# Kernel tuning notes

Hardware: AMD Instinct MI355X
Metric: run time of the kernel (lower is better)

The kernel has to match this reference:

```python
import jax, jax.numpy as jnp
import numpy as np

GRID = 12  # sqrt(144), seq_len = 144 fixed by w_g shape


def _relative_position(n: int) -> jnp.ndarray:
    # grid cell centers for an n x n grid, flattened row-major -> (n*n,)
    idx = np.arange(n * n)
    row, col = idx // n, idx % n
    cx = (col + 0.5) / n  # (x_min + x_max)/2 with x_min=col/n, x_max=(col+1)/n
    cy = (row + 0.5) / n
    dx = cx[:, None] - cx[None, :]
    dy = cy[:, None] - cy[None, :]
    ax = np.sign(dx) * 0.5
    ay = np.sign(dy) * 0.5
    dx = np.abs(np.log(np.abs(dx) + 0.5))
    dy = np.abs(np.log(np.abs(dy) + 0.5))
    # cat along leading dim then permute(1,2,0) == stack last-dim in order (dx,dy,ax,ay)
    pos = np.stack([dx, dy, ax, ay], axis=-1).astype(np.float32)  # (S,S,4)
    return jnp.asarray(pos)


def setup_inputs() -> dict:
    key = jax.random.key(0)
    ks = jax.random.split(key, 9)
    B, S, D = 128, GRID * GRID, 1024
    sc = 1.0 / np.sqrt(D)
    return {
        "query": jax.random.normal(ks[0], (B, S, D), jnp.float32),
        "key": jax.random.normal(ks[1], (B, S, D), jnp.float32),
        "value": jax.random.normal(ks[2], (B, S, D), jnp.float32),
        "Wq": jax.random.normal(ks[3], (D, D), jnp.float32) * sc,
        "bq": jnp.zeros((D,), jnp.float32),
        "Wk": jax.random.normal(ks[4], (D, D), jnp.float32) * sc,
        "bk": jnp.zeros((D,), jnp.float32),
        "Wv": jax.random.normal(ks[5], (D, D), jnp.float32) * sc,
        "bv": jnp.zeros((D,), jnp.float32),
        "Wlin": jax.random.normal(ks[6], (D, 4), jnp.float32) * 0.5,
        "w_g": jax.random.normal(ks[7], (S, D, 1), jnp.float32) * sc,
    }


def reference(query, key, value, Wq, bq, Wk, bk, Wv, bv, Wlin, w_g):
    d_model = query.shape[-1]
    # QKV projections + ReLU activation (dropout is identity at eval)
    q = jax.nn.relu(jnp.einsum("bsd,ed->bse", query, Wq) + bq)
    k = jax.nn.relu(jnp.einsum("bsd,ed->bse", key, Wk) + bk)
    v = jax.nn.relu(jnp.einsum("bsd,ed->bse", value, Wv) + bv)
    # raw scores: (B, S, S)
    att = jnp.einsum("bsd,btd->bst", q, k) * (d_model ** -0.5)
    # relative-position bias: (S, S, 4) -> linear -> relu -> per-row w_g -> relu
    pos = _relative_position(GRID)
    rp = jax.nn.relu(jnp.einsum("stf,df->std", pos, Wlin))  # (S, S, D)
    rp = jax.nn.relu(jnp.einsum("std,sdo->sto", rp, w_g)[..., 0])  # (S, S)
    att = jax.nn.softmax(att + rp[None, :, :], axis=-1)
    return jnp.einsum("bst,btd->bsd", att, v)
```

## Files before the change

### kernel.cpp

```cpp
#include <hip/hip_runtime.h>
#include <hip/hip_fp16.h>

#define DEV __device__ __forceinline__

using half8 = __attribute__((ext_vector_type(8))) _Float16;
using half4 = __attribute__((ext_vector_type(4))) _Float16;
using f32x4 = __attribute__((ext_vector_type(4))) float;

DEV void gload_lds16(const void* g, void* l) {
  __builtin_amdgcn_global_load_lds((const __attribute__((address_space(1))) unsigned int*)g,
                                   (__attribute__((address_space(3))) unsigned int*)l,
                                   16, 0, 0);
}

DEV f32x4 mfma16x32(half8 a, half8 b, f32x4 c) {
  return __builtin_amdgcn_mfma_f32_16x16x32_f16(a, b, c, 0, 0, 0);
}

DEV void conv2048(const float* __restrict__ s, _Float16* __restrict__ d, int t) {
  int i = t * 8;
  float4 a = *(const float4*)(s + i);
  float4 b = *(const float4*)(s + i + 4);
  half8 h;
  h[0] = (_Float16)a.x; h[1] = (_Float16)a.y; h[2] = (_Float16)a.z; h[3] = (_Float16)a.w;
  h[4] = (_Float16)b.x; h[5] = (_Float16)b.y; h[6] = (_Float16)b.z; h[7] = (_Float16)b.w;
  *(half8*)(d + i) = h;
}

DEV void rp_body(const float* __restrict__ Wlin, const float* __restrict__ wg,
                 float* __restrict__ rp, int s, int t) {
  if (t >= 144) return;
  int rs = s / 12, cs = s % 12, rt = t / 12, ct = t % 12;
  float dx = (cs - ct) / 12.f, dy = (rs - rt) / 12.f;
  float ax = (dx > 0.f) ? 0.5f : (dx < 0.f ? -0.5f : 0.f);
  float ay = (dy > 0.f) ? 0.5f : (dy < 0.f ? -0.5f : 0.f);
  float lx = fabsf(logf(fabsf(dx) + 0.5f));
  float ly = fabsf(logf(fabsf(dy) + 0.5f));
  float a0 = 0.f, a1 = 0.f, a2 = 0.f, a3 = 0.f;
  const float* wgs = wg + s * 1024;
  for (int d = 0; d < 1024; d += 4) {
#pragma unroll
    for (int u = 0; u < 4; ++u) {
      float4 w = *(const float4*)(Wlin + (d + u) * 4);
      float dot = lx * w.x + ly * w.y + ax * w.z + ay * w.w;
      dot = dot > 0.f ? dot : 0.f;
      float p = dot * wgs[d + u];
      if (u == 0) a0 += p; else if (u == 1) a1 += p; else if (u == 2) a2 += p; else a3 += p;
    }
  }
  float acc = (a0 + a1) + (a2 + a3);
  rp[s * 144 + t] = acc > 0.f ? acc : 0.f;
}

__global__ void prep_all(const float* __restrict__ query, const float* __restrict__ key,
                         const float* __restrict__ value, _Float16* __restrict__ ia,
                         _Float16* __restrict__ ib, _Float16* __restrict__ ic,
                         const float* __restrict__ Wq, const float* __restrict__ Wk,
                         const float* __restrict__ Wv, _Float16* __restrict__ Wqb,
                         _Float16* __restrict__ Wkb, _Float16* __restrict__ Wvb,
                         const float* __restrict__ Wlin, const float* __restrict__ wg,
                         float* __restrict__ rp, _Float16* __restrict__ vt) {
  int id = blockIdx.x, t = threadIdx.x;
  if (id < 144) {
    rp_body(Wlin, wg, rp, id, t);
  } else if (id < 656) {
    int i = (id - 144) * 256 + t;
    _Float16* p = vt + (size_t)i * 160 + 144;
    *(half8*)p = (half8){};
    *(half8*)(p + 8) = (half8){};
  } else if (id < 2192) {
    int id3 = id - 656;
    int z = id3 >> 9, r = id3 & 511;
    const float* s = z == 0 ? Wq : (z == 1 ? Wk : Wv);
    _Float16* d = z == 0 ? Wqb : (z == 1 ? Wkb : Wvb);
    conv2048(s + r * 2048, d + r * 2048, t);
  } else {
    int id4 = id - 2192;
    int z = id4 / 9216, r = id4 % 9216;
    const float* s = z == 0 ? query : (z == 1 ? key : value);
    _Float16* d = z == 0 ? ia : (z == 1 ? ib : ic);
    conv2048(s + (size_t)r * 2048, d + (size_t)r * 2048, t);
  }
}

__global__ void prep_small(const float* __restrict__ Wq, const float* __restrict__ Wk,
                           const float* __restrict__ Wv, _Float16* __restrict__ Wqb,
                           _Float16* __restrict__ Wkb, _Float16* __restrict__ Wvb,
                           const float* __restrict__ Wlin, const float* __restrict__ wg,
                           float* __restrict__ rp, _Float16* __restrict__ vt) {
  int id = blockIdx.x, t = threadIdx.x;
  if (id < 144) {
    rp_body(Wlin, wg, rp, id, t);
  } else if (id < 656) {
    int i = (id - 144) * 256 + t;
    _Float16* p = vt + (size_t)i * 160 + 144;
    *(half8*)p = (half8){};
    *(half8*)(p + 8) = (half8){};
  } else {
    int id3 = id - 656;
    int z = id3 >> 9, r = id3 & 511;
    const float* s = z == 0 ? Wq : (z == 1 ? Wk : Wv);
    _Float16* d = z == 0 ? Wqb : (z == 1 ? Wkb : Wvb);
    conv2048(s + r * 2048, d + r * 2048, t);
  }
}

__global__ void conv3_f32_f16(const float* __restrict__ s0, const float* __restrict__ s1,
                              const float* __restrict__ s2, _Float16* __restrict__ d0,
                              _Float16* __restrict__ d1, _Float16* __restrict__ d2, int n) {
  const float* s = blockIdx.z == 0 ? s0 : (blockIdx.z == 1 ? s1 : s2);
  _Float16* d = blockIdx.z == 0 ? d0 : (blockIdx.z == 1 ? d1 : d2);
  int i = blockIdx.x * 2048;
  if (i >= n) return;
  conv2048(s + i, d + i, (int)threadIdx.x);
}

__global__ __launch_bounds__(256, 2) void gemm_proj(
    const _Float16* __restrict__ a0q, const _Float16* __restrict__ a1q,
    const _Float16* __restrict__ a2q, const _Float16* __restrict__ w0q,
    const _Float16* __restrict__ w1q, const _Float16* __restrict__ w2q,
    const float* __restrict__ bi0, const float* __restrict__ bi1,
    const float* __restrict__ bi2, _Float16* __restrict__ c0q,
    _Float16* __restrict__ c1q, _Float16* __restrict__ c2q,
    _Float16* __restrict__ vtp, int vtz) {
  const _Float16* A = blockIdx.z == 0 ? a0q : (blockIdx.z == 1 ? a1q : a2q);
  const _Float16* W = blockIdx.z == 0 ? w0q : (blockIdx.z == 1 ? w1q : w2q);
  const float* bias = blockIdx.z == 0 ? bi0 : (blockIdx.z == 1 ? bi1 : bi2);
  _Float16* C = blockIdx.z == 0 ? c0q : (blockIdx.z == 1 ? c1q : c2q);

  __shared__ __align__(16) char lds[79872];
  int tid = threadIdx.x, wid = tid >> 6, lane = tid & 63;
  int lin = blockIdx.y * 8 + blockIdx.x;
  int local = lin >> 3;
  int mt = (lin & 7) * 8 + (local >> 3), nt = local & 7;
  int m0 = mt * 288, n0 = nt * 128;

  int r4l = lane >> 2, c4 = lane & 3;
  int cg8 = ((c4 + (r4l >> 1)) & 3) * 8;
  int lr = lane & 15, lg = lane >> 4;
  int rdoff = lr * 64 + ((lg - (lr >> 1)) & 3) * 16;

  const _Float16* gp[7];
#pragma unroll
  for (int c = 0; c < 7; ++c) {
    int q = c * 4 + wid;
    if (q < 26)
      gp[c] = (q < 18) ? A + (size_t)(m0 + q * 16 + r4l) * 1024 + cg8
                       : W + (size_t)(n0 + (q - 18) * 16 + r4l) * 1024 + cg8;
    else
      gp[c] = A;
  }
  char *sl0 = lds, *sl1 = lds + 26624, *sl2 = lds + 53248;
  auto issue = [&](char* slot) {
#pragma unroll
    for (int c = 0; c < 7; ++c) {
      if (c * 4 + wid < 26) { gload_lds16(gp[c], slot + (c * 4 + wid) * 1024); gp[c] += 32; }
    }
  };
  issue(sl0);
  issue(sl1);
  f32x4 acc[9][4] = {};
  int abase = (wid >> 1) * 9216, bbase = 18432 + (wid & 1) * 4096;
  for (int t = 0; t < 32; ++t) {
    if (wid < 2) asm volatile("s_waitcnt vmcnt(7)" ::: "memory");
    else         asm volatile("s_waitcnt vmcnt(6)" ::: "memory");
    __builtin_amdgcn_s_barrier();
    __builtin_amdgcn_sched_barrier(0);
    issue(sl2);
    half8 a[9], b[4];
#pragma unroll
    for (int i = 0; i < 9; ++i) a[i] = *(const half8*)(sl0 + abase + i * 1024 + rdoff);
#pragma unroll
    for (int j = 0; j < 4; ++j) b[j] = *(const half8*)(sl0 + bbase + j * 1024 + rdoff);
#pragma unroll
    for (int i = 0; i < 9; ++i)
#pragma unroll
      for (int j = 0; j < 4; ++j)
        acc[i][j] = mfma16x32(b[j], a[i], acc[i][j]);
    char* tmp = sl0; sl0 = sl1; sl1 = sl2; sl2 = tmp;
  }
  int wm = (wid >> 1) * 144, wn = (wid & 1) * 64;
  bool tov = (vtp != nullptr) && ((int)blockIdx.z == vtz);
#pragma unroll
  for (int i = 0; i < 9; ++i) {
    int row = m0 + wm + i * 16 + lr;
#pragma unroll
    for (int j = 0; j < 4; ++j) {
      int col = n0 + wn + j * 16 + lg * 4;
      float4 b4 = *(const float4*)(bias + col);
      half4 h;
      float v0 = acc[i][j][0] + b4.x; h[0] = (_Float16)(v0 > 0.f ? v0 : 0.f);
      float v1 = acc[i][j][1] + b4.y; h[1] = (_Float16)(v1 > 0.f ? v1 : 0.f);
      float v2 = acc[i][j][2] + b4.z; h[2] = (_Float16)(v2 > 0.f ? v2 : 0.f);
      float v3 = acc[i][j][3] + b4.w; h[3] = (_Float16)(v3 > 0.f ? v3 : 0.f);
      if (tov) {
        int bb = row / 144, ss = row - bb * 144;
        _Float16* vb = vtp + (size_t)(bb * 1024 + col) * 160 + ss;
        vb[0] = h[0]; vb[160] = h[1]; vb[320] = h[2]; vb[480] = h[3];
      } else {
        *(half4*)(C + (size_t)row * 1024 + col) = h;
      }
    }
  }
}

__global__ __launch_bounds__(256) void attn1_kernel(const _Float16* __restrict__ q,
                                                    const _Float16* __restrict__ k,
                                                    const float* __restrict__ rp,
                                                    _Float16* __restrict__ Pg,
                                                    float* __restrict__ sums_g) {
  __shared__ __align__(16) char lds[53248];
  float* sc = (float*)lds;
  _Float16* P = (_Float16*)(lds + 36864);
  float* sums = (float*)(lds + 52992);

  int tid = threadIdx.x, wid = tid >> 6, lane = tid & 63;
  int lin = blockIdx.y * 3 + blockIdx.x;
  int swz = (lin & 7) * 48 + (lin >> 3);
  int mt3 = swz % 3, b = swz / 3;
  int m0 = mt3 * 48;
  const int nstart_t[4] = {0, 3, 5, 7};
  const int ncnt_t[4]   = {3, 2, 2, 2};
  int ns = nstart_t[wid], nc = ncnt_t[wid];
  int r4l = lane >> 2, c4 = lane & 3;
  int cg8 = ((c4 + (r4l >> 1)) & 3) * 8;
  int lr = lane & 15, lg = lane >> 4;
  int rdoff = lr * 64 + ((lg - (lr >> 1)) & 3) * 16;

  {
    char *sl0 = lds, *sl1 = lds + 12288, *sl2 = lds + 24576;
    const _Float16* g1[3];
#pragma unroll
    for (int c = 0; c < 3; ++c) {
      int qq = c * 4 + wid;
      g1[c] = (qq < 3) ? q + (size_t)(b * 144 + m0 + qq * 16 + r4l) * 1024 + cg8
                       : k + (size_t)(b * 144 + (qq - 3) * 16 + r4l) * 1024 + cg8;
    }
    auto issue1 = [&](char* slot) {
#pragma unroll
      for (int c = 0; c < 3; ++c) {
        gload_lds16(g1[c], slot + (c * 4 + wid) * 1024);
        g1[c] += 32;
      }
    };
    issue1(sl0);
    issue1(sl1);
    f32x4 acc[3][3] = {};
    for (int t = 0; t < 32; ++t) {
      asm volatile("s_waitcnt vmcnt(3)" ::: "memory");
      __builtin_amdgcn_sched_barrier(0);
      __builtin_amdgcn_s_barrier();
      __builtin_amdgcn_sched_barrier(0);
      issue1(sl2);
      half8 af[3], bf[3];
#pragma unroll
      for (int i = 0; i < 3; ++i)
        af[i] = *(const half8*)(sl0 + i * 1024 + rdoff);
#pragma unroll
      for (int j = 0; j < 3; ++j)
        if (j < nc)
          bf[j] = *(const half8*)(sl0 + (3 + ns + j) * 1024 + rdoff);
#pragma unroll
      for (int i = 0; i < 3; ++i)
#pragma unroll
        for (int j = 0; j < 3; ++j)
          if (j < nc)
            acc[i][j] = mfma16x32(bf[j], af[i], acc[i][j]);
      char* tmp = sl0; sl0 = sl1; sl1 = sl2; sl2 = tmp;
    }
    asm volatile("s_waitcnt vmcnt(0)" ::: "memory");
    __syncthreads();
    const float scale = 0.03125f;
#pragma unroll
    for (int i = 0; i < 3; ++i) {
      int qrow = i * 16 + lr;
#pragma unroll
      for (int j = 0; j < 3; ++j)
        if (j < nc) {
          int kc0 = (ns + j) * 16 + lg * 4;
          float4 rr = *(const float4*)(rp + (m0 + qrow) * 144 + kc0);
          f32x4 vs;
          vs[0] = acc[i][j][0] * scale + rr.x;
          vs[1] = acc[i][j][1] * scale + rr.y;
          vs[2] = acc[i][j][2] * scale + rr.z;
          vs[3] = acc[i][j][3] * scale + rr.w;
          *(f32x4*)(sc + qrow * 152 + kc0) = vs;
        }
    }
  }
  __syncthreads();

  if (tid < 192) {
    int r = tid >> 2, qd = tid & 3;
    int cb = qd * 36;
    float m = -1e30f;
    for (int c2 = 0; c2 < 36; ++c2) m = fmaxf(m, sc[r * 152 + cb + c2]);
    m = fmaxf(m, __shfl_xor(m, 1));
    m = fmaxf(m, __shfl_xor(m, 2));
    float s = 0.f;
    for (int c2 = 0; c2 < 36; ++c2) {
      float e = __expf(sc[r * 152 + cb + c2] - m);
      s += e;
      P[r * 168 + cb + c2] = (_Float16)e;
    }
    s += __shfl_xor(s, 1);
    s += __shfl_xor(s, 2);
    if (qd == 0) sums[r] = s;
  }
  if (tid < 96) {
    int r = tid >> 1, c0 = 144 + (tid & 1) * 8;
    *(half8*)(P + r * 168 + c0) = (half8){};
  }
  __syncthreads();

  {
    int bt = b * 3 + mt3;
    _Float16* Pgb = Pg + (size_t)bt * 48 * 160;
    for (int idx = tid; idx < 960; idx += 256) {
      int r = idx / 20, c = idx % 20;
      *(half8*)(Pgb + r * 160 + c * 8) = *(const half8*)(P + r * 168 + c * 8);
    }
    if (tid < 48) sums_g[bt * 48 + tid] = sums[tid];
  }
}

__global__ __launch_bounds__(256) void attn_pv(const _Float16* __restrict__ Pg,
                                               const float* __restrict__ sums_g,
                                               const _Float16* __restrict__ vt,
                                               float* __restrict__ out) {
  __shared__ __align__(16) char lds[32768];
  int tid = threadIdx.x, wid = tid >> 6, lane = tid & 63;
  int lin = blockIdx.y * 12 + blockIdx.x;
  int swz = (lin & 7) * 192 + (lin >> 3);
  int bt = swz >> 2, nq = swz & 3;
  int b = bt / 3, m0 = (bt % 3) * 48;
  int r4l = lane >> 2, c4 = lane & 3;
  int cg8 = ((c4 + (r4l >> 1)) & 3) * 8;
  int lr = lane & 15, lg = lane >> 4;
  int rdoff = lr * 64 + ((lg - (lr >> 1)) & 3) * 16;

  char *s0p = lds, *s1p = lds + 16384;
  auto issue = [&](int it, char* slot) {
#pragma unroll
    for (int c = 0; c < 4; ++c) {
      int ch = c * 4 + wid;
      gload_lds16(vt + (size_t)(b * 1024 + nq * 256 + ch * 16 + r4l) * 160 + it * 32 + cg8,
                  slot + ch * 1024);
    }
  };
  issue(0, s0p);
  f32x4 o[3][4] = {};
  for (int it = 0; it < 5; ++it) {
    asm volatile("s_waitcnt vmcnt(0)" ::: "memory");
    __builtin_amdgcn_sched_barrier(0);
    __builtin_amdgcn_s_barrier();
    __builtin_amdgcn_sched_barrier(0);
    if (it < 4) issue(it + 1, (it & 1) ? s0p : s1p);
    char* sb = (it & 1) ? s1p : s0p;
    int k0 = it * 32;
    half8 af[3], bf[4];
#pragma unroll
    for (int i = 0; i < 3; ++i)
      af[i] = *(const half8*)(Pg + ((size_t)bt * 48 + i * 16 + lr) * 160 + k0 + lg * 8);
#pragma unroll
    for (int j = 0; j < 4; ++j)
      bf[j] = *(const half8*)(sb + (wid * 4 + j) * 1024 + rdoff);
#pragma unroll
    for (int i = 0; i < 3; ++i)
#pragma unroll
      for (int j = 0; j < 4; ++j)
        o[i][j] = mfma16x32(bf[j], af[i], o[i][j]);
  }
#pragma unroll
  for (int i = 0; i < 3; ++i) {
    int row = i * 16 + lr;
    float inv = 1.f / sums_g[bt * 48 + row];
#pragma unroll
    for (int j = 0; j < 4; ++j) {
      f32x4 vo;
      vo[0] = o[i][j][0] * inv; vo[1] = o[i][j][1] * inv;
      vo[2] = o[i][j][2] * inv; vo[3] = o[i][j][3] * inv;
      *(f32x4*)(out + (size_t)(b * 144 + m0 + row) * 1024 + nq * 256 + wid * 64 + j * 16 + lg * 4) = vo;
    }
  }
}

extern "C" void kernel_launch(void* const* d_in, const int* in_sizes, int n_in,
                              void* d_out, int out_size, void* d_ws, size_t ws_size,
                              hipStream_t stream) {
  const float* query = (const float*)d_in[0];
  const float* key   = (const float*)d_in[1];
  const float* value = (const float*)d_in[2];
  const float* Wq    = (const float*)d_in[3];
  const float* bq    = (const float*)d_in[4];
  const float* Wk    = (const float*)d_in[5];
  const float* bk    = (const float*)d_in[6];
  const float* Wv    = (const float*)d_in[7];
  const float* bv    = (const float*)d_in[8];
  const float* Wlin  = (const float*)d_in[9];
  const float* wg    = (const float*)d_in[10];
  float* out = (float*)d_out;

  char* ws = (char*)d_ws;
  const size_t NQKV = (size_t)18432 * 1024;
  const size_t NVT  = (size_t)131072 * 160;
  _Float16* Wqb = (_Float16*)(ws);
  _Float16* Wkb = (_Float16*)(ws + (2u << 20));
  _Float16* Wvb = (_Float16*)(ws + (4u << 20));
  float*    rp  = (float*)(ws + (6u << 20));
  _Float16* qp  = (_Float16*)(ws + (6u << 20) + 131072);
  _Float16* kp  = qp + NQKV;
  _Float16* vt  = kp + NQKV;

  dim3 a1grid(3, 128), pvgrid(12, 128);

  if (ws_size >= 238000000ull) {
    _Float16* ia = vt + NVT + 32768;
    _Float16* ib = ia + NQKV;
    _Float16* ic = ib + NQKV;
    _Float16* Pg = ia;
    float* sums_g = (float*)((char*)ia + (6u << 20));
    prep_all<<<29840, 256, 0, stream>>>(query, key, value, ia, ib, ic,
                                        Wq, Wk, Wv, Wqb, Wkb, Wvb,
                                        Wlin, wg, rp, vt);
    gemm_proj<<<dim3(8, 64, 3), 256, 0, stream>>>(ia, ib, ic, Wqb, Wkb, Wvb,
                                                  bq, bk, bv, qp, kp, kp ,
                                                  vt, 2);
    attn1_kernel<<<a1grid, 256, 0, stream>>>(qp, kp, rp, Pg, sums_g);
    attn_pv<<<pvgrid, 256, 0, stream>>>(Pg, sums_g, vt, out);
  } else {
    _Float16* inb = vt + NVT;
    _Float16* Pg = inb;
    float* sums_g = (float*)((char*)inb + (6u << 20));
    prep_small<<<2192, 256, 0, stream>>>(Wq, Wk, Wv, Wqb, Wkb, Wvb, Wlin, wg, rp, vt);
    conv3_f32_f16<<<dim3((int)(NQKV / 2048), 1, 1), 256, 0, stream>>>(
        query, query, query, inb, inb, inb, (int)NQKV);
    gemm_proj<<<dim3(8, 64, 1), 256, 0, stream>>>(inb, inb, inb, Wqb, Wqb, Wqb,
                                                  bq, bq, bq, qp, qp, qp, nullptr, -1);
    conv3_f32_f16<<<dim3((int)(NQKV / 2048), 1, 1), 256, 0, stream>>>(
        key, key, key, inb, inb, inb, (int)NQKV);
    gemm_proj<<<dim3(8, 64, 1), 256, 0, stream>>>(inb, inb, inb, Wkb, Wkb, Wkb,
                                                  bk, bk, bk, kp, kp, kp, nullptr, -1);
    conv3_f32_f16<<<dim3((int)(NQKV / 2048), 1, 1), 256, 0, stream>>>(
        value, value, value, inb, inb, inb, (int)NQKV);
    gemm_proj<<<dim3(8, 64, 1), 256, 0, stream>>>(inb, inb, inb, Wvb, Wvb, Wvb,
                                                  bv, bv, bv, qp , qp, qp,
                                                  vt, 0);
    attn1_kernel<<<a1grid, 256, 0, stream>>>(qp, kp, rp, Pg, sums_g);
    attn_pv<<<pvgrid, 256, 0, stream>>>(Pg, sums_g, vt, out);
  }
}
```

Baseline: 272.5 us.

## Co-schedule V projection GEMM with attention-score kernel in one launch

```diff
diff --git a/kernel.cpp b/kernel.cpp
--- a/kernel.cpp
+++ b/kernel.cpp
@@ -115,22 +115,10 @@
   conv2048(s + i, d + i, (int)threadIdx.x);
 }
 
-__global__ __launch_bounds__(256, 2) void gemm_proj(
-    const _Float16* __restrict__ a0q, const _Float16* __restrict__ a1q,
-    const _Float16* __restrict__ a2q, const _Float16* __restrict__ w0q,
-    const _Float16* __restrict__ w1q, const _Float16* __restrict__ w2q,
-    const float* __restrict__ bi0, const float* __restrict__ bi1,
-    const float* __restrict__ bi2, _Float16* __restrict__ c0q,
-    _Float16* __restrict__ c1q, _Float16* __restrict__ c2q,
-    _Float16* __restrict__ vtp, int vtz) {
-  const _Float16* A = blockIdx.z == 0 ? a0q : (blockIdx.z == 1 ? a1q : a2q);
-  const _Float16* W = blockIdx.z == 0 ? w0q : (blockIdx.z == 1 ? w1q : w2q);
-  const float* bias = blockIdx.z == 0 ? bi0 : (blockIdx.z == 1 ? bi1 : bi2);
-  _Float16* C = blockIdx.z == 0 ? c0q : (blockIdx.z == 1 ? c1q : c2q);
-
-  __shared__ __align__(16) char lds[79872];
+DEV void gemm_body(char* lds, int lin, const _Float16* __restrict__ A,
+                   const _Float16* __restrict__ W, const float* __restrict__ bias,
+                   _Float16* __restrict__ C, _Float16* __restrict__ vtp) {
   int tid = threadIdx.x, wid = tid >> 6, lane = tid & 63;
-  int lin = blockIdx.y * 8 + blockIdx.x;
   int local = lin >> 3;
   int mt = (lin & 7) * 8 + (local >> 3), nt = local & 7;
   int m0 = mt * 288, n0 = nt * 128;
@@ -180,7 +168,7 @@
     char* tmp = sl0; sl0 = sl1; sl1 = sl2; sl2 = tmp;
   }
   int wm = (wid >> 1) * 144, wn = (wid & 1) * 64;
-  bool tov = (vtp != nullptr) && ((int)blockIdx.z == vtz);
+  bool tov = (vtp != nullptr);
 #pragma unroll
   for (int i = 0; i < 9; ++i) {
     int row = m0 + wm + i * 16 + lr;
@@ -204,18 +192,32 @@
   }
 }
 
-__global__ __launch_bounds__(256) void attn1_kernel(const _Float16* __restrict__ q,
-                                                    const _Float16* __restrict__ k,
-                                                    const float* __restrict__ rp,
-                                                    _Float16* __restrict__ Pg,
-                                                    float* __restrict__ sums_g) {
-  __shared__ __align__(16) char lds[53248];
+__global__ __launch_bounds__(256, 2) void gemm_proj(
+    const _Float16* __restrict__ a0q, const _Float16* __restrict__ a1q,
+    const _Float16* __restrict__ a2q, const _Float16* __restrict__ w0q,
+    const _Float16* __restrict__ w1q, const _Float16* __restrict__ w2q,
+    const float* __restrict__ bi0, const float* __restrict__ bi1,
+    const float* __restrict__ bi2, _Float16* __restrict__ c0q,
+    _Float16* __restrict__ c1q, _Float16* __restrict__ c2q,
+    _Float16* __restrict__ vtp, int vtz) {
+  const _Float16* A = blockIdx.z == 0 ? a0q : (blockIdx.z == 1 ? a1q : a2q);
+  const _Float16* W = blockIdx.z == 0 ? w0q : (blockIdx.z == 1 ? w1q : w2q);
+  const float* bias = blockIdx.z == 0 ? bi0 : (blockIdx.z == 1 ? bi1 : bi2);
+  _Float16* C = blockIdx.z == 0 ? c0q : (blockIdx.z == 1 ? c1q : c2q);
+  __shared__ __align__(16) char lds[79872];
+  int lin = blockIdx.y * 8 + blockIdx.x;
+  bool tov = (vtp != nullptr) && ((int)blockIdx.z == vtz);
+  gemm_body(lds, lin, A, W, bias, C, tov ? vtp : nullptr);
+}
+
+DEV void attn1_body(char* lds, int lin, const _Float16* __restrict__ q,
+                    const _Float16* __restrict__ k, const float* __restrict__ rp,
+                    _Float16* __restrict__ Pg, float* __restrict__ sums_g) {
   float* sc = (float*)lds;
   _Float16* P = (_Float16*)(lds + 36864);
   float* sums = (float*)(lds + 52992);
 
   int tid = threadIdx.x, wid = tid >> 6, lane = tid & 63;
-  int lin = blockIdx.y * 3 + blockIdx.x;
   int swz = (lin & 7) * 48 + (lin >> 3);
   int mt3 = swz % 3, b = swz / 3;
   int m0 = mt3 * 48;
@@ -324,6 +326,28 @@
   }
 }
 
+__global__ __launch_bounds__(256) void attn1_kernel(const _Float16* __restrict__ q,
+                                                    const _Float16* __restrict__ k,
+                                                    const float* __restrict__ rp,
+                                                    _Float16* __restrict__ Pg,
+                                                    float* __restrict__ sums_g) {
+  __shared__ __align__(16) char lds[53248];
+  int lin = blockIdx.y * 3 + blockIdx.x;
+  attn1_body(lds, lin, q, k, rp, Pg, sums_g);
+}
+
+__global__ __launch_bounds__(256, 2) void gemm_v_attn1(
+    const _Float16* __restrict__ ic, const _Float16* __restrict__ Wvb,
+    const float* __restrict__ bv, _Float16* __restrict__ vt,
+    const _Float16* __restrict__ qp, const _Float16* __restrict__ kp,
+    const float* __restrict__ rp, _Float16* __restrict__ Pg,
+    float* __restrict__ sums_g) {
+  __shared__ __align__(16) char lds[79872];
+  int id = blockIdx.x, r7 = id % 7, g = id / 7;
+  if (r7 < 4) gemm_body(lds, g * 4 + r7, ic, Wvb, bv, vt , vt);
+  else        attn1_body(lds, g * 3 + (r7 - 4), qp, kp, rp, Pg, sums_g);
+}
+
 __global__ __launch_bounds__(256) void attn_pv(const _Float16* __restrict__ Pg,
                                                const float* __restrict__ sums_g,
                                                const _Float16* __restrict__ vt,
@@ -423,10 +447,10 @@
     prep_all<<<29840, 256, 0, stream>>>(query, key, value, ia, ib, ic,
                                         Wq, Wk, Wv, Wqb, Wkb, Wvb,
                                         Wlin, wg, rp, vt);
-    gemm_proj<<<dim3(8, 64, 3), 256, 0, stream>>>(ia, ib, ic, Wqb, Wkb, Wvb,
-                                                  bq, bk, bv, qp, kp, kp ,
-                                                  vt, 2);
-    attn1_kernel<<<a1grid, 256, 0, stream>>>(qp, kp, rp, Pg, sums_g);
+    gemm_proj<<<dim3(8, 64, 2), 256, 0, stream>>>(ia, ib, ib , Wqb, Wkb, Wkb,
+                                                  bq, bk, bk, qp, kp, kp,
+                                                  nullptr, -1);
+    gemm_v_attn1<<<896, 256, 0, stream>>>(ic, Wvb, bv, vt, qp, kp, rp, Pg, sums_g);
     attn_pv<<<pvgrid, 256, 0, stream>>>(Pg, sums_g, vt, out);
   } else {
     _Float16* inb = vt + NVT;
```

New measurement: 294.9 us. +8.2%, slower.
